# Optimization experiments

Hardware: AMD Instinct MI355X
Metric: run time of the kernel (lower is better)

## Reference

```python
import jax, jax.numpy as jnp
import numpy as np

NUM_HEADS = 12


def _qkv_split(x, qkv_w, num_heads):
    B, N, C = x.shape
    hd = C // num_heads
    qkv = (x @ qkv_w).reshape(B, N, 3, num_heads, hd)
    qkv = jnp.transpose(qkv, (2, 0, 3, 1, 4))  # [3, B, H, N, hd]
    return qkv[0], qkv[1], qkv[2]


def setup_inputs() -> dict:
    key = jax.random.key(0)
    k1, k2, k3, k4 = jax.random.split(key, 4)
    B, N, C = 8, 1024, 768
    s = 0.02
    return {
        "x1": jax.random.normal(k1, (B, N, C), dtype=jnp.float32),
        "x2": jax.random.normal(k2, (B, N, C), dtype=jnp.float32),
        "qkv_w": jax.random.normal(k3, (C, 3 * C), dtype=jnp.float32) * s,
        "proj_w": jax.random.normal(k4, (C, C), dtype=jnp.float32) * s,
        "proj_b": jnp.zeros((C,), dtype=jnp.float32),
    }


def reference(x1, x2, qkv_w, proj_w, proj_b):
    B, N, C = x1.shape
    H = NUM_HEADS
    hd = C // H
    scale = hd ** (-0.5)

    q, k, v = _qkv_split(x1, qkv_w, H)    # each [B, H, N, hd]
    q2, k2, v2 = _qkv_split(x2, qkv_w, H)

    # self-attention branch: q attends to k/v (from x1)
    attn1 = jax.nn.softmax(jnp.einsum('bhqd,bhkd->bhqk', q, k) * scale, axis=-1)
    o1 = jnp.einsum('bhqk,bhkd->bhqd', attn1, v)

    # cross-attention branch: same q attends to k2/v2 (from x2)
    attn2 = jax.nn.softmax(jnp.einsum('bhqd,bhkd->bhqk', q, k2) * scale, axis=-1)
    o2 = jnp.einsum('bhqk,bhkd->bhqd', attn2, v2)

    o1 = jnp.transpose(o1, (0, 2, 1, 3)).reshape(B, N, C) @ proj_w + proj_b
    o2 = jnp.transpose(o2, (0, 2, 1, 3)).reshape(B, N, C) @ proj_w + proj_b
    return (o1, o2)
```

## Files before the change

kernel.cpp:

```cpp
#include <hip/hip_runtime.h>
#include <hip/hip_bf16.h>

#define N_ 1024
#define C_ 768
#define H_ 12

typedef unsigned short u16;
typedef __attribute__((ext_vector_type(8))) short bf16x8;
typedef __attribute__((ext_vector_type(4))) float f32x4;
typedef __attribute__((ext_vector_type(16))) float f32x16;

#define MFMA16(a, b, c) __builtin_amdgcn_mfma_f32_16x16x32_bf16(a, b, c, 0, 0, 0)
#define MFMA32(a, b, c) __builtin_amdgcn_mfma_f32_32x32x16_bf16(a, b, c, 0, 0, 0)

#define GLDS16(gp, lp) __builtin_amdgcn_global_load_lds(                     \
    (const __attribute__((address_space(1))) void*)(gp),                     \
    (__attribute__((address_space(3))) void*)(lp), 16, 0, 0)

__device__ __forceinline__ u16 f2bu(float x) {
    unsigned u = __float_as_uint(x);
    unsigned r = (u + 0x7fffu + ((u >> 16) & 1u)) >> 16;
    return (u16)r;
}

__device__ __forceinline__ unsigned cvtpk(float a, float b) {
    unsigned d;
    asm("v_cvt_pk_bf16_f32 %0, %1, %2" : "=v"(d) : "v"(a), "v"(b));
    return d;
}

__global__ __launch_bounds__(256) void cvt_x(
    const float* __restrict__ x1, const float* __restrict__ x2,
    u16* __restrict__ d1, u16* __restrict__ d2)
{
    const size_t G = 786432;
    for (size_t i = (size_t)blockIdx.x * 256 + threadIdx.x; i < 2 * G;
         i += (size_t)gridDim.x * 256) {
        const float* src = (i < G) ? x1 : x2;
        u16* dst = (i < G) ? d1 : d2;
        size_t g = (i < G) ? i : i - G;
        float4 f0 = ((const float4*)src)[g * 2];
        float4 f1 = ((const float4*)src)[g * 2 + 1];
        ushort4 lo, hi;
        lo.x = f2bu(f0.x); lo.y = f2bu(f0.y); lo.z = f2bu(f0.z); lo.w = f2bu(f0.w);
        hi.x = f2bu(f1.x); hi.y = f2bu(f1.y); hi.z = f2bu(f1.z); hi.w = f2bu(f1.w);
        ((ushort4*)dst)[g * 2] = lo;
        ((ushort4*)dst)[g * 2 + 1] = hi;
    }
}

__global__ __launch_bounds__(256) void tr_cvt(
    const float* __restrict__ W, u16* __restrict__ WT, int R, int CC)
{
    __shared__ float t[32][33];
    const int tx = threadIdx.x & 31, ty = threadIdx.x >> 5;
    const int c0 = blockIdx.x * 32, r0 = blockIdx.y * 32;
#pragma unroll
    for (int i = 0; i < 4; ++i) {
        int r = ty + i * 8;
        t[r][tx] = W[(size_t)(r0 + r) * CC + c0 + tx];
    }
    __syncthreads();
#pragma unroll
    for (int i = 0; i < 4; ++i) {
        int c = ty + i * 8;
        WT[(size_t)(c0 + c) * R + r0 + tx] = f2bu(t[tx][c]);
    }
}

__global__ __launch_bounds__(512) void qkv_gemm(
    const u16* __restrict__ A1, const u16* __restrict__ A2,
    const u16* __restrict__ BT, u16* __restrict__ qd,
    u16* __restrict__ k1d, u16* __restrict__ k2d,
    u16* __restrict__ vt1d, u16* __restrict__ vt2d)
{
    __shared__ u16 As[2][128 * 64];
    __shared__ u16 Bs[2][128 * 64];
    const int tid = threadIdx.x;
    const int w = tid >> 6, lane = tid & 63;
    const int c31 = lane & 31, h = lane >> 5;
    const int wm = w >> 2, wn = w & 3;
    const int id = blockIdx.x;
    const int xcd = id & 7, j = id >> 3;
    const int by = xcd * 8 + j / 30;
    const int bx = j % 30;
    const bool first = bx < 18;
    const u16* A = first ? A1 : A2;
    const int row0 = by * 128;
    const int nc0 = first ? bx * 128 : 768 + (bx - 18) * 128;

    f32x16 acc[2];
#pragma unroll
    for (int i = 0; i < 2; ++i)
#pragma unroll
        for (int e = 0; e < 16; ++e) acc[i][e] = 0.f;

    const int srow = tid >> 3;
    const int sch = ((tid & 7) ^ (srow & 7)) * 8;
    int aoff[2], boff[2];
#pragma unroll
    for (int i = 0; i < 2; ++i) {
        int row = i * 64 + srow;
        aoff[i] = (row0 + row) * C_ + sch;
        boff[i] = (nc0 + row) * C_ + sch;
    }
    char* adst0 = (char*)&As[0][0] + w * 1024;
    char* bdst0 = (char*)&Bs[0][0] + w * 1024;
    auto stage = [&](int buf, int k0) {
#pragma unroll
        for (int i = 0; i < 2; ++i) {
            GLDS16(A + aoff[i] + k0, adst0 + buf * 16384 + i * 8192);
            GLDS16(BT + boff[i] + k0, bdst0 + buf * 16384 + i * 8192);
        }
    };

    const int ra0 = wm * 64 + c31, ra1 = ra0 + 32;
    const int rb0 = wn * 32 + c31;

    stage(0, 0);
    for (int kt = 0; kt < 12; ++kt) {
        const int buf = kt & 1;
        if (kt < 11) {
            stage(buf ^ 1, (kt + 1) * 64);
            asm volatile("s_waitcnt vmcnt(4)" ::: "memory");
        } else {
            asm volatile("s_waitcnt vmcnt(0)" ::: "memory");
        }
        __builtin_amdgcn_s_barrier();
        const char* abase = (const char*)&As[0][0] + buf * 16384;
        const char* bbase = (const char*)&Bs[0][0] + buf * 16384;
#pragma unroll
        for (int kh = 0; kh < 4; ++kh) {
            bf16x8 a0 = *(const bf16x8*)(abase + ra0 * 128 + (((2 * kh + h) ^ (ra0 & 7)) * 16));
            bf16x8 a1 = *(const bf16x8*)(abase + ra1 * 128 + (((2 * kh + h) ^ (ra1 & 7)) * 16));
            bf16x8 b0 = *(const bf16x8*)(bbase + rb0 * 128 + (((2 * kh + h) ^ (rb0 & 7)) * 16));
            acc[0] = MFMA32(a0, b0, acc[0]);
            acc[1] = MFMA32(a1, b0, acc[1]);
        }
        asm volatile("" ::: "memory");
        __builtin_amdgcn_s_barrier();
    }

    u16* kd  = first ? k1d : k2d;
    u16* vtd = first ? vt1d : vt2d;
    const int col = nc0 + wn * 32 + c31;
    const int sec = col / C_;
    const int hh = (col % C_) >> 6;
    const int d = col & 63;
    const float scl = (sec == 0) ? 0.180336877f : 1.0f;
#pragma unroll
    for (int mt = 0; mt < 2; ++mt)
#pragma unroll
        for (int r = 0; r < 16; ++r) {
            int row = row0 + wm * 64 + mt * 32 + (r & 3) + 8 * (r >> 2) + 4 * h;
            int b = row >> 10, n = row & 1023;
            u16 val = f2bu(acc[mt][r] * scl);
            size_t bh = (size_t)(b * H_ + hh);
            if (sec == 0)      qd[(bh * N_ + n) * 64 + d] = val;
            else if (sec == 1) kd[(bh * N_ + n) * 64 + d] = val;
            else {
                int nprm = (n & ~63) | (((n & 15) << 2) | ((n >> 4) & 3));
                vtd[(bh * 64 + d) * N_ + nprm] = val;
            }
        }
}

__global__ __launch_bounds__(512) void proj_gemm(
    const u16* __restrict__ A1, const u16* __restrict__ A2,
    const u16* __restrict__ BT, const float* __restrict__ bias,
    float* __restrict__ out)
{
    __shared__ u16 As[2][128 * 64];
    __shared__ u16 Bs[2][128 * 64];
    const int tid = threadIdx.x;
    const int w = tid >> 6, lane = tid & 63;
    const int c31 = lane & 31, h = lane >> 5;
    const int wm = w >> 2, wn = w & 3;
    const int id = blockIdx.x;
    const int xcd = id & 7, j = id >> 3;
    const int byg = xcd * 16 + j / 6;
    const int sel = byg >> 6;
    const u16* A = sel ? A2 : A1;
    float* op = out + (size_t)sel * 8192 * C_;
    const int row0 = (byg & 63) * 128;
    const int nc0 = (j % 6) * 128;

    f32x16 acc[2];
#pragma unroll
    for (int i = 0; i < 2; ++i)
#pragma unroll
        for (int e = 0; e < 16; ++e) acc[i][e] = 0.f;

    const int srow = tid >> 3;
    const int sch = ((tid & 7) ^ (srow & 7)) * 8;
    int aoff[2], boff[2];
#pragma unroll
    for (int i = 0; i < 2; ++i) {
        int row = i * 64 + srow;
        aoff[i] = (row0 + row) * C_ + sch;
        boff[i] = (nc0 + row) * C_ + sch;
    }
    char* adst0 = (char*)&As[0][0] + w * 1024;
    char* bdst0 = (char*)&Bs[0][0] + w * 1024;
    auto stage = [&](int buf, int k0) {
#pragma unroll
        for (int i = 0; i < 2; ++i) {
            GLDS16(A + aoff[i] + k0, adst0 + buf * 16384 + i * 8192);
            GLDS16(BT + boff[i] + k0, bdst0 + buf * 16384 + i * 8192);
        }
    };

    const int ra0 = wm * 64 + c31, ra1 = ra0 + 32;
    const int rb0 = wn * 32 + c31;

    stage(0, 0);
    for (int kt = 0; kt < 12; ++kt) {
        const int buf = kt & 1;
        if (kt < 11) {
            stage(buf ^ 1, (kt + 1) * 64);
            asm volatile("s_waitcnt vmcnt(4)" ::: "memory");
        } else {
            asm volatile("s_waitcnt vmcnt(0)" ::: "memory");
        }
        __builtin_amdgcn_s_barrier();
        const char* abase = (const char*)&As[0][0] + buf * 16384;
        const char* bbase = (const char*)&Bs[0][0] + buf * 16384;
#pragma unroll
        for (int kh = 0; kh < 4; ++kh) {
            bf16x8 a0 = *(const bf16x8*)(abase + ra0 * 128 + (((2 * kh + h) ^ (ra0 & 7)) * 16));
            bf16x8 a1 = *(const bf16x8*)(abase + ra1 * 128 + (((2 * kh + h) ^ (ra1 & 7)) * 16));
            bf16x8 b0 = *(const bf16x8*)(bbase + rb0 * 128 + (((2 * kh + h) ^ (rb0 & 7)) * 16));
            acc[0] = MFMA32(a0, b0, acc[0]);
            acc[1] = MFMA32(a1, b0, acc[1]);
        }
        asm volatile("" ::: "memory");
        __builtin_amdgcn_s_barrier();
    }

    const int col = nc0 + wn * 32 + c31;
#pragma unroll
    for (int mt = 0; mt < 2; ++mt)
#pragma unroll
        for (int r = 0; r < 16; ++r) {
            int row = row0 + wm * 64 + mt * 32 + (r & 3) + 8 * (r >> 2) + 4 * h;
            op[(size_t)row * C_ + col] = acc[mt][r] + bias[col];
        }
}

__global__ __launch_bounds__(256) void attn_mfma(
    const u16* __restrict__ Q,
    const u16* __restrict__ K1, const u16* __restrict__ VT1,
    const u16* __restrict__ K2, const u16* __restrict__ VT2,
    u16* __restrict__ O1, u16* __restrict__ O2)
{
    __shared__ u16 Ks[2][64 * 64];
    __shared__ u16 Vs[2][64 * 64];
    __shared__ u16 Ps[4][32 * 72];
    const int tid = threadIdx.x;
    const int w = tid >> 6, lane = tid & 63;
    const int g = lane >> 4, ln = lane & 15;
    const int id = blockIdx.x;
    const int xcd = id & 7, j = id >> 3;
    const int unit = j >> 3;
    const int qb = j & 7;
    const int br = unit >= 12;
    const int bh = xcd * 12 + (br ? unit - 12 : unit);
    const int qw = qb * 128 + w * 32;
    const size_t hb = (size_t)bh * N_ * 64;

    const u16* Kb = (br ? K2 : K1) + hb;
    const u16* Vb = (br ? VT2 : VT1) + hb;
    const u16* Qb = Q + hb;
    u16* O        = br ? O2 : O1;

    bf16x8 qf[2][2];
#pragma unroll
    for (int mt = 0; mt < 2; ++mt)
#pragma unroll
        for (int s = 0; s < 2; ++s)
            qf[mt][s] = *(const bf16x8*)(Qb + (size_t)(qw + mt * 16 + ln) * 64 + s * 32 + g * 8);

    f32x4 o[2][4];
    float lsum[2][4];
#pragma unroll
    for (int mt = 0; mt < 2; ++mt) {
#pragma unroll
        for (int t = 0; t < 4; ++t) o[mt][t] = (f32x4){0.f, 0.f, 0.f, 0.f};
#pragma unroll
        for (int r = 0; r < 4; ++r) lsum[mt][r] = 0.f;
    }

    auto stage = [&](int buf, int key0) {
#pragma unroll
        for (int i = 0; i < 2; ++i) {
            int L = (i * 256 + tid) * 16;
            int row = L >> 7;
            int sw = (((L >> 4) & 7) ^ (row & 7)) * 8;
            GLDS16(Kb + (size_t)(key0 + row) * 64 + sw,
                   (char*)&Ks[buf][0] + i * 4096 + w * 1024);
            GLDS16(Vb + (size_t)row * N_ + key0 + sw,
                   (char*)&Vs[buf][0] + i * 4096 + w * 1024);
        }
    };

    u16* pw = &Ps[w][0];
    const int r7 = ln & 7;

    stage(0, 0);
    __syncthreads();
    for (int kt = 0; kt < 16; ++kt) {
        const int buf = kt & 1;
        if (kt < 15) stage(buf ^ 1, (kt + 1) * 64);
        const char* kbase = (const char*)&Ks[buf][0];
        f32x4 st[2][4];
#pragma unroll
        for (int nt = 0; nt < 4; ++nt) {
            const char* krow = kbase + (nt * 16 + ln) * 128;
            bf16x8 kf0 = *(const bf16x8*)(krow + ((g ^ r7) * 16));
            bf16x8 kf1 = *(const bf16x8*)(krow + (((g + 4) ^ r7) * 16));
#pragma unroll
            for (int mt = 0; mt < 2; ++mt) {
                f32x4 z = (f32x4){0.f, 0.f, 0.f, 0.f};
                z = MFMA16(qf[mt][0], kf0, z);
                z = MFMA16(qf[mt][1], kf1, z);
                st[mt][nt] = z;
            }
        }
#pragma unroll
        for (int mt = 0; mt < 2; ++mt)
#pragma unroll
            for (int r = 0; r < 4; ++r) {
                float p0 = __builtin_amdgcn_exp2f(st[mt][0][r]);
                float p1 = __builtin_amdgcn_exp2f(st[mt][1][r]);
                float p2 = __builtin_amdgcn_exp2f(st[mt][2][r]);
                float p3 = __builtin_amdgcn_exp2f(st[mt][3][r]);
                lsum[mt][r] += (p0 + p1) + (p2 + p3);
                uint2 pk;
                pk.x = cvtpk(p0, p1);
                pk.y = cvtpk(p2, p3);
                int prow = mt * 16 + g * 4 + r;
                *(uint2*)((char*)pw + prow * 144 + ln * 8) = pk;
            }
        const char* vbase = (const char*)&Vs[buf][0];
#pragma unroll
        for (int s = 0; s < 2; ++s) {
            bf16x8 pa[2];
            pa[0] = *(const bf16x8*)((const char*)pw + (0 + ln) * 144 + s * 64 + g * 16);
            pa[1] = *(const bf16x8*)((const char*)pw + (16 + ln) * 144 + s * 64 + g * 16);
#pragma unroll
            for (int t = 0; t < 4; ++t) {
                bf16x8 vf = *(const bf16x8*)(vbase + (t * 16 + ln) * 128 + (((s * 4 + g) ^ r7) * 16));
#pragma unroll
                for (int mt = 0; mt < 2; ++mt) o[mt][t] = MFMA16(pa[mt], vf, o[mt][t]);
            }
        }
        __syncthreads();
    }
    const int b = bh / H_, h = bh % H_;
#pragma unroll
    for (int mt = 0; mt < 2; ++mt)
#pragma unroll
        for (int r = 0; r < 4; ++r) {
            float ls = lsum[mt][r];
#pragma unroll
            for (int off = 8; off; off >>= 1) ls += __shfl_xor(ls, off);
            float inv = 1.f / ls;
            int n = qw + mt * 16 + g * 4 + r;
            u16* orow = O + ((size_t)(b * N_) + n) * C_ + h * 64 + ln;
#pragma unroll
            for (int t = 0; t < 4; ++t)
                orow[t * 16] = f2bu(o[mt][t][r] * inv);
        }
}

extern "C" void kernel_launch(void* const* d_in, const int* in_sizes, int n_in,
                              void* d_out, int out_size, void* d_ws, size_t ws_size,
                              hipStream_t stream) {
    const float* x1     = (const float*)d_in[0];
    const float* x2     = (const float*)d_in[1];
    const float* qkv_w  = (const float*)d_in[2];
    const float* proj_w = (const float*)d_in[3];
    const float* proj_b = (const float*)d_in[4];
    float* out = (float*)d_out;

    u16* ws = (u16*)d_ws;
    const size_t SZ = (size_t)8 * H_ * N_ * 64;
    u16* wqkvT  = ws;
    u16* wprojT = wqkvT + (size_t)2304 * 768;
    u16* q      = wprojT + (size_t)768 * 768;
    u16* k1     = q + SZ;
    u16* vT1    = k1 + SZ;
    u16* slotA  = vT1 + SZ;
    u16* vT2    = slotA + SZ;
    u16* slotB  = vT2 + SZ;
    u16* x1c = slotA, *o2p = slotA;
    u16* x2c = slotB, *o1p = slotB;
    u16* k2buf = (u16*)(out + SZ);

    cvt_x<<<2048, 256, 0, stream>>>(x1, x2, x1c, x2c);
    tr_cvt<<<dim3(72, 24), 256, 0, stream>>>(qkv_w, wqkvT, C_, 3 * C_);
    tr_cvt<<<dim3(24, 24), 256, 0, stream>>>(proj_w, wprojT, C_, C_);
    qkv_gemm<<<1920, 512, 0, stream>>>(x1c, x2c, wqkvT, q, k1, k2buf, vT1, vT2);
    attn_mfma<<<1536, 256, 0, stream>>>(q, k1, vT1, k2buf, vT2, o1p, o2p);
    proj_gemm<<<768, 512, 0, stream>>>(o1p, o2p, wprojT, proj_b, out);
}
```

Measured before the change: 206.4 us.

## Merge prep kernels into one launch and raise wave priority around MFMA loops

Combines the input conversion and both weight transpose-convert kernels into a single launch, with block ranges dispatching to each job. This removes two kernel launches and their gaps. Separately, wraps the MFMA inner loops in the QKV GEMM, projection GEMM and attention kernel with s_setprio raise/lower so that waves issuing matrix ops get scheduling priority. The priority hints may help or hurt interleaving with memory-issuing waves.

```diff
diff --git a/kernel.cpp b/kernel.cpp
--- a/kernel.cpp
+++ b/kernel.cpp
@@ -29,42 +29,49 @@
     return d;
 }
 
-__global__ __launch_bounds__(256) void cvt_x(
+__global__ __launch_bounds__(256) void prep(
     const float* __restrict__ x1, const float* __restrict__ x2,
-    u16* __restrict__ d1, u16* __restrict__ d2)
+    const float* __restrict__ qkv_w, const float* __restrict__ proj_w,
+    u16* __restrict__ d1, u16* __restrict__ d2,
+    u16* __restrict__ wqkvT, u16* __restrict__ wprojT)
 {
-    const size_t G = 786432;
-    for (size_t i = (size_t)blockIdx.x * 256 + threadIdx.x; i < 2 * G;
-         i += (size_t)gridDim.x * 256) {
-        const float* src = (i < G) ? x1 : x2;
-        u16* dst = (i < G) ? d1 : d2;
-        size_t g = (i < G) ? i : i - G;
-        float4 f0 = ((const float4*)src)[g * 2];
-        float4 f1 = ((const float4*)src)[g * 2 + 1];
-        ushort4 lo, hi;
-        lo.x = f2bu(f0.x); lo.y = f2bu(f0.y); lo.z = f2bu(f0.z); lo.w = f2bu(f0.w);
-        hi.x = f2bu(f1.x); hi.y = f2bu(f1.y); hi.z = f2bu(f1.z); hi.w = f2bu(f1.w);
-        ((ushort4*)dst)[g * 2] = lo;
-        ((ushort4*)dst)[g * 2 + 1] = hi;
-    }
-}
-
-__global__ __launch_bounds__(256) void tr_cvt(
-    const float* __restrict__ W, u16* __restrict__ WT, int R, int CC)
-{
-    __shared__ float t[32][33];
-    const int tx = threadIdx.x & 31, ty = threadIdx.x >> 5;
-    const int c0 = blockIdx.x * 32, r0 = blockIdx.y * 32;
-#pragma unroll
-    for (int i = 0; i < 4; ++i) {
-        int r = ty + i * 8;
-        t[r][tx] = W[(size_t)(r0 + r) * CC + c0 + tx];
-    }
-    __syncthreads();
-#pragma unroll
-    for (int i = 0; i < 4; ++i) {
-        int c = ty + i * 8;
-        WT[(size_t)(c0 + c) * R + r0 + tx] = f2bu(t[tx][c]);
+    const int bid = blockIdx.x;
+    if (bid < 2304) {
+        __shared__ float t[32][33];
+        const int txi = bid % 96, ty = bid / 96;
+        const bool isq = txi < 72;
+        const float* W = isq ? qkv_w : proj_w;
+        u16* WT = isq ? wqkvT : wprojT;
+        const int CC = isq ? 2304 : 768;
+        const int c0 = (isq ? txi : txi - 72) * 32;
+        const int r0 = ty * 32;
+        const int tx = threadIdx.x & 31, tyy = threadIdx.x >> 5;
+#pragma unroll
+        for (int i = 0; i < 4; ++i) {
+            int r = tyy + i * 8;
+            t[r][tx] = W[(size_t)(r0 + r) * CC + c0 + tx];
+        }
+        __syncthreads();
+#pragma unroll
+        for (int i = 0; i < 4; ++i) {
+            int c = tyy + i * 8;
+            WT[(size_t)(c0 + c) * 768 + r0 + tx] = f2bu(t[tx][c]);
+        }
+    } else {
+        const size_t G = 786432;
+        for (size_t i = (size_t)(bid - 2304) * 256 + threadIdx.x; i < 2 * G;
+             i += (size_t)1536 * 256) {
+            const float* src = (i < G) ? x1 : x2;
+            u16* dst = (i < G) ? d1 : d2;
+            size_t g = (i < G) ? i : i - G;
+            float4 f0 = ((const float4*)src)[g * 2];
+            float4 f1 = ((const float4*)src)[g * 2 + 1];
+            ushort4 lo, hi;
+            lo.x = f2bu(f0.x); lo.y = f2bu(f0.y); lo.z = f2bu(f0.z); lo.w = f2bu(f0.w);
+            hi.x = f2bu(f1.x); hi.y = f2bu(f1.y); hi.z = f2bu(f1.z); hi.w = f2bu(f1.w);
+            ((ushort4*)dst)[g * 2] = lo;
+            ((ushort4*)dst)[g * 2 + 1] = hi;
+        }
     }
 }
 
@@ -129,6 +136,7 @@
         __builtin_amdgcn_s_barrier();
         const char* abase = (const char*)&As[0][0] + buf * 16384;
         const char* bbase = (const char*)&Bs[0][0] + buf * 16384;
+        __builtin_amdgcn_s_setprio(1);
 #pragma unroll
         for (int kh = 0; kh < 4; ++kh) {
             bf16x8 a0 = *(const bf16x8*)(abase + ra0 * 128 + (((2 * kh + h) ^ (ra0 & 7)) * 16));
@@ -137,6 +145,7 @@
             acc[0] = MFMA32(a0, b0, acc[0]);
             acc[1] = MFMA32(a1, b0, acc[1]);
         }
+        __builtin_amdgcn_s_setprio(0);
         asm volatile("" ::: "memory");
         __builtin_amdgcn_s_barrier();
     }
@@ -225,6 +234,7 @@
         __builtin_amdgcn_s_barrier();
         const char* abase = (const char*)&As[0][0] + buf * 16384;
         const char* bbase = (const char*)&Bs[0][0] + buf * 16384;
+        __builtin_amdgcn_s_setprio(1);
 #pragma unroll
         for (int kh = 0; kh < 4; ++kh) {
             bf16x8 a0 = *(const bf16x8*)(abase + ra0 * 128 + (((2 * kh + h) ^ (ra0 & 7)) * 16));
@@ -233,6 +243,7 @@
             acc[0] = MFMA32(a0, b0, acc[0]);
             acc[1] = MFMA32(a1, b0, acc[1]);
         }
+        __builtin_amdgcn_s_setprio(0);
         asm volatile("" ::: "memory");
         __builtin_amdgcn_s_barrier();
     }
@@ -313,6 +324,7 @@
         if (kt < 15) stage(buf ^ 1, (kt + 1) * 64);
         const char* kbase = (const char*)&Ks[buf][0];
         f32x4 st[2][4];
+        __builtin_amdgcn_s_setprio(1);
 #pragma unroll
         for (int nt = 0; nt < 4; ++nt) {
             const char* krow = kbase + (nt * 16 + ln) * 128;
@@ -326,6 +338,7 @@
                 st[mt][nt] = z;
             }
         }
+        __builtin_amdgcn_s_setprio(0);
 #pragma unroll
         for (int mt = 0; mt < 2; ++mt)
 #pragma unroll
@@ -342,6 +355,7 @@
                 *(uint2*)((char*)pw + prow * 144 + ln * 8) = pk;
             }
         const char* vbase = (const char*)&Vs[buf][0];
+        __builtin_amdgcn_s_setprio(1);
 #pragma unroll
         for (int s = 0; s < 2; ++s) {
             bf16x8 pa[2];
@@ -354,6 +368,7 @@
                 for (int mt = 0; mt < 2; ++mt) o[mt][t] = MFMA16(pa[mt], vf, o[mt][t]);
             }
         }
+        __builtin_amdgcn_s_setprio(0);
         __syncthreads();
     }
     const int b = bh / H_, h = bh % H_;
@@ -397,9 +412,7 @@
     u16* x2c = slotB, *o1p = slotB;
     u16* k2buf = (u16*)(out + SZ);
 
-    cvt_x<<<2048, 256, 0, stream>>>(x1, x2, x1c, x2c);
-    tr_cvt<<<dim3(72, 24), 256, 0, stream>>>(qkv_w, wqkvT, C_, 3 * C_);
-    tr_cvt<<<dim3(24, 24), 256, 0, stream>>>(proj_w, wprojT, C_, C_);
+    prep<<<3840, 256, 0, stream>>>(x1, x2, qkv_w, proj_w, x1c, x2c, wqkvT, wprojT);
     qkv_gemm<<<1920, 512, 0, stream>>>(x1c, x2c, wqkvT, q, k1, k2buf, vT1, vT2);
     attn_mfma<<<1536, 256, 0, stream>>>(q, k1, vT1, k2buf, vT2, o1p, o2p);
     proj_gemm<<<768, 512, 0, stream>>>(o1p, o2p, wprojT, proj_b, out);
```

Measured after the change: 210.0 us. About the same (+1.7%).
